# Performance work log

Measured on AMD Instinct MI355X. Metric: run time of the kernel, lower is better.

Reference implementation:

```python
import jax, jax.numpy as jnp
import numpy as np

N_NODES = 50000
N_EDGES = 800000
IN_CH, HID, OUT_CH, N_LAYERS = 512, 64, 40, 64
ALPHA, THETA = 0.5, 1.0


def setup_inputs() -> dict:
    key = jax.random.key(0)
    ks = jax.random.split(key, 6)
    x = jax.random.normal(ks[0], (N_NODES, IN_CH), dtype=jnp.float32)
    edge_index = jax.random.randint(ks[1], (2, N_EDGES), 0, N_NODES, dtype=jnp.int64)
    lin1_w = jax.random.normal(ks[2], (IN_CH, HID), dtype=jnp.float32) * (1.0 / np.sqrt(IN_CH))
    lin1_b = jnp.zeros((HID,), dtype=jnp.float32)
    conv_w = jax.random.normal(ks[3], (N_LAYERS, HID, HID), dtype=jnp.float32) * (1.0 / np.sqrt(HID))
    lin2_w = jax.random.normal(ks[4], (HID, OUT_CH), dtype=jnp.float32) * (1.0 / np.sqrt(HID))
    lin2_b = jnp.zeros((OUT_CH,), dtype=jnp.float32)
    return {"x": x, "edge_index": edge_index, "lin1_w": lin1_w, "lin1_b": lin1_b,
            "conv_w": conv_w, "lin2_w": lin2_w, "lin2_b": lin2_b}


def reference(x, edge_index, lin1_w, lin1_b, conv_w, lin2_w, lin2_b):
    # Eval-mode forward (dropout is identity).
    N = x.shape[0]
    # gcn_norm: add self-loops, symmetric sqrt-degree normalization
    loop = jnp.arange(N, dtype=edge_index.dtype)
    src = jnp.concatenate([edge_index[0], loop])  # [E+N]
    dst = jnp.concatenate([edge_index[1], loop])
    w = jnp.ones(src.shape[0], dtype=x.dtype)
    deg = jax.ops.segment_sum(w, dst, num_segments=N)
    dinv = jnp.where(deg > 0, jax.lax.rsqrt(jnp.maximum(deg, 1e-12)), 0.0)
    norm = (dinv[src] * dinv[dst])[:, None]  # [E+N, 1]

    h = jax.nn.relu(x @ lin1_w + lin1_b)  # [N, HID]
    x0 = h
    L = conv_w.shape[0]
    betas = jnp.log(THETA / jnp.arange(1, L + 1, dtype=x.dtype) + 1.0)

    def step(h, wb):
        W, beta = wb
        # sparse neighbor aggregation: out[i] = sum_{j->i} norm * h[j]
        agg = jax.ops.segment_sum(h[src] * norm, dst, num_segments=N)
        z = (1.0 - ALPHA) * agg + ALPHA * x0            # initial residual
        z = (1.0 - beta) * z + beta * (z @ W)           # identity mapping
        return jax.nn.relu(z), None

    h, _ = jax.lax.scan(step, h, (conv_w, betas))
    out = h @ lin2_w + lin2_b
    return jax.nn.log_softmax(out, axis=1)
```

## Files before the change

### kernel.cpp

```cpp
#include <hip/hip_runtime.h>
#include <hip/hip_bf16.h>
#include <hip/hip_fp16.h>
#include <math.h>

#define HID 64

union HU { __half h; unsigned short u; };
__device__ inline float h2f(unsigned short u) { HU x; x.u = u; return __half2float(x.h); }
__device__ inline unsigned short f2h(float f) { HU x; x.h = __float2half(f); return x.u; }


__global__ void count_kernel(const int* __restrict__ dst, int* __restrict__ cnt, int E, int N) {
    int e = blockIdx.x * blockDim.x + threadIdx.x;
    if (e < E) {
        int d = dst[e];
        if ((unsigned)d < (unsigned)N) atomicAdd(&cnt[d], 1);
    }
}

__global__ void dinv_kernel(const int* __restrict__ cnt, float* __restrict__ dinv, int n) {
    int i = blockIdx.x * blockDim.x + threadIdx.x;
    if (i < n) {
        float deg = (float)(cnt[i] + 1);
        dinv[i] = rsqrtf(deg);
    }
}

__global__ __launch_bounds__(1024) void scanA_kernel(const int* __restrict__ cnt,
        int* __restrict__ offs, int* __restrict__ bsum, int n) {
    __shared__ int buf[1024];
    int tid = threadIdx.x;
    int i = blockIdx.x * 1024 + tid;
    int v = (i < n) ? cnt[i] : 0;
    buf[tid] = v;
    __syncthreads();
    for (int off = 1; off < 1024; off <<= 1) {
        int t = (tid >= off) ? buf[tid - off] : 0;
        __syncthreads();
        buf[tid] += t;
        __syncthreads();
    }
    if (i < n) offs[i] = buf[tid] - v;
    if (tid == 1023) bsum[blockIdx.x] = buf[1023];
}

__global__ __launch_bounds__(1024) void scanB_kernel(int* __restrict__ bsum, int nb) {
    __shared__ int buf[1024];
    int tid = threadIdx.x;
    int v = (tid < nb) ? bsum[tid] : 0;
    buf[tid] = v;
    __syncthreads();
    for (int off = 1; off < 1024; off <<= 1) {
        int t = (tid >= off) ? buf[tid - off] : 0;
        __syncthreads();
        buf[tid] += t;
        __syncthreads();
    }
    if (tid < nb) bsum[tid] = buf[tid] - v;
    if (tid == nb - 1) bsum[nb] = buf[tid];
}

__global__ __launch_bounds__(1024) void scanC_kernel(int* __restrict__ offs,
        const int* __restrict__ bsum, int n, int nb) {
    int i = blockIdx.x * 1024 + threadIdx.x;
    if (i < n) offs[i] += bsum[i >> 10];
    if (i == 0) offs[n] = bsum[nb];
}

__global__ void fill_kernel(const int* __restrict__ src, const int* __restrict__ dst,
                            const int* __restrict__ offs, int* __restrict__ cursor,
                            const float* __restrict__ dinv,
                            int2* __restrict__ pack, int E, int N) {
    int e = blockIdx.x * blockDim.x + threadIdx.x;
    if (e < E) {
        int s = src[e], d = dst[e];
        if ((unsigned)s < (unsigned)N && (unsigned)d < (unsigned)N) {
            int pos = atomicAdd(&cursor[d], 1);
            int j = offs[d] + pos;
            if ((unsigned)j < (unsigned)E)
                pack[j] = make_int2(s, __float_as_int(dinv[s] * dinv[d]));
        }
    }
}


__global__ __launch_bounds__(256) void lin1_kernel(const float* __restrict__ x,
        const float* __restrict__ W, const float* __restrict__ b,
        float* __restrict__ out32, unsigned short* __restrict__ out16, int n) {
    const int BM = 64, BK = 32;
    __shared__ float As[BM][BK + 1];
    __shared__ float Ws[BK][64];
    int tid = threadIdx.x;
    int row0 = blockIdx.x * BM;
    int tx = tid & 15, ty = tid >> 4;
    float acc[4][4] = {};

    int ar = tid >> 3, ac4 = tid & 7;
    int wr = tid >> 4, wc4 = tid & 15;
    float4 a_pf[2], w_pf[2];

    #pragma unroll
    for (int rr = 0; rr < 2; rr++) {
        int row = row0 + ar + rr * 32;
        a_pf[rr] = make_float4(0.f, 0.f, 0.f, 0.f);
        if (row < n) a_pf[rr] = *(const float4*)&x[(size_t)row * 512 + ac4 * 4];
        w_pf[rr] = *(const float4*)&W[(size_t)(wr + rr * 16) * 64 + wc4 * 4];
    }

    for (int k0 = 0; k0 < 512; k0 += BK) {
        #pragma unroll
        for (int rr = 0; rr < 2; rr++) {
            As[ar + rr * 32][ac4 * 4 + 0] = a_pf[rr].x;
            As[ar + rr * 32][ac4 * 4 + 1] = a_pf[rr].y;
            As[ar + rr * 32][ac4 * 4 + 2] = a_pf[rr].z;
            As[ar + rr * 32][ac4 * 4 + 3] = a_pf[rr].w;
            *(float4*)&Ws[wr + rr * 16][wc4 * 4] = w_pf[rr];
        }
        __syncthreads();
        int k1 = k0 + BK;
        if (k1 < 512) {
            #pragma unroll
            for (int rr = 0; rr < 2; rr++) {
                int row = row0 + ar + rr * 32;
                a_pf[rr] = make_float4(0.f, 0.f, 0.f, 0.f);
                if (row < n) a_pf[rr] = *(const float4*)&x[(size_t)row * 512 + k1 + ac4 * 4];
                w_pf[rr] = *(const float4*)&W[(size_t)(k1 + wr + rr * 16) * 64 + wc4 * 4];
            }
        }
        #pragma unroll
        for (int kk = 0; kk < BK; kk++) {
            float a0 = As[ty * 4 + 0][kk];
            float a1 = As[ty * 4 + 1][kk];
            float a2 = As[ty * 4 + 2][kk];
            float a3 = As[ty * 4 + 3][kk];
            float4 w = *(float4*)&Ws[kk][tx * 4];
            acc[0][0] += a0 * w.x; acc[0][1] += a0 * w.y; acc[0][2] += a0 * w.z; acc[0][3] += a0 * w.w;
            acc[1][0] += a1 * w.x; acc[1][1] += a1 * w.y; acc[1][2] += a1 * w.z; acc[1][3] += a1 * w.w;
            acc[2][0] += a2 * w.x; acc[2][1] += a2 * w.y; acc[2][2] += a2 * w.z; acc[2][3] += a2 * w.w;
            acc[3][0] += a3 * w.x; acc[3][1] += a3 * w.y; acc[3][2] += a3 * w.z; acc[3][3] += a3 * w.w;
        }
        __syncthreads();
    }
    #pragma unroll
    for (int i = 0; i < 4; i++) {
        int row = row0 + ty * 4 + i;
        if (row < n) {
            #pragma unroll
            for (int j = 0; j < 4; j++) {
                int col = tx * 4 + j;
                float v = fmaxf(acc[i][j] + b[col], 0.f);
                out32[(size_t)row * 64 + col] = v;
                out16[(size_t)row * 64 + col] = f2h(v);
            }
        }
    }
}


__global__ __launch_bounds__(256) void layer_kernel(
        const ushort4* __restrict__ h16, const float4* __restrict__ x04,
        unsigned short* __restrict__ h_out,
        const int* __restrict__ rowptr, const int2* __restrict__ pack,
        const float* __restrict__ dinv,
        const float* __restrict__ W, float beta, int n) {
    __shared__ float Wsh[HID * HID];
    __shared__ float4 zt[4][HID];
    int tid = threadIdx.x;
    for (int i = tid; i < HID * HID / 4; i += 256)
        ((float4*)Wsh)[i] = ((const float4*)W)[i];
    __syncthreads();
    int lane = tid & 63, wave = tid >> 6;
    int g = lane >> 4;
    int c = lane & 15;
    float omb = 1.0f - beta;

    for (int base = (blockIdx.x * 4 + wave) * 4; base < n; base += gridDim.x * 16) {
        int node = base + g;
        float4 acc = make_float4(0.f, 0.f, 0.f, 0.f);
        if (node < n) {
            float di = dinv[node];
            float d2 = di * di;
            ushort4 sv = h16[(size_t)node * 16 + c];
            acc.x = d2 * h2f(sv.x); acc.y = d2 * h2f(sv.y);
            acc.z = d2 * h2f(sv.z); acc.w = d2 * h2f(sv.w);
            int e0 = rowptr[node];
            int deg = rowptr[node + 1] - e0;
            int e = 0;
            for (; e + 4 <= deg; e += 4) {
                int2 p0 = pack[e0 + e + 0];
                int2 p1 = pack[e0 + e + 1];
                int2 p2 = pack[e0 + e + 2];
                int2 p3 = pack[e0 + e + 3];
                ushort4 v0 = h16[(size_t)p0.x * 16 + c];
                ushort4 v1 = h16[(size_t)p1.x * 16 + c];
                ushort4 v2 = h16[(size_t)p2.x * 16 + c];
                ushort4 v3 = h16[(size_t)p3.x * 16 + c];
                float n0 = __int_as_float(p0.y), n1 = __int_as_float(p1.y);
                float n2 = __int_as_float(p2.y), n3 = __int_as_float(p3.y);
                acc.x += n0 * h2f(v0.x) + n1 * h2f(v1.x) + n2 * h2f(v2.x) + n3 * h2f(v3.x);
                acc.y += n0 * h2f(v0.y) + n1 * h2f(v1.y) + n2 * h2f(v2.y) + n3 * h2f(v3.y);
                acc.z += n0 * h2f(v0.z) + n1 * h2f(v1.z) + n2 * h2f(v2.z) + n3 * h2f(v3.z);
                acc.w += n0 * h2f(v0.w) + n1 * h2f(v1.w) + n2 * h2f(v2.w) + n3 * h2f(v3.w);
            }
            for (; e < deg; e++) {
                int2 p = pack[e0 + e];
                ushort4 v = h16[(size_t)p.x * 16 + c];
                float nv = __int_as_float(p.y);
                acc.x += nv * h2f(v.x); acc.y += nv * h2f(v.y);
                acc.z += nv * h2f(v.z); acc.w += nv * h2f(v.w);
            }
            float4 x0v = x04[(size_t)node * 16 + c];
            acc.x = 0.5f * acc.x + 0.5f * x0v.x;
            acc.y = 0.5f * acc.y + 0.5f * x0v.y;
            acc.z = 0.5f * acc.z + 0.5f * x0v.z;
            acc.w = 0.5f * acc.w + 0.5f * x0v.w;
        }
        {
            float* zf = (float*)&zt[wave][0];
            zf[(4 * c + 0) * 4 + g] = acc.x;
            zf[(4 * c + 1) * 4 + g] = acc.y;
            zf[(4 * c + 2) * 4 + g] = acc.z;
            zf[(4 * c + 3) * 4 + g] = acc.w;
        }
        float4 mv = make_float4(0.f, 0.f, 0.f, 0.f);
        #pragma unroll 8
        for (int k = 0; k < HID; k++) {
            float4 zk = zt[wave][k];
            float wk = Wsh[k * HID + lane];
            mv.x += zk.x * wk; mv.y += zk.y * wk;
            mv.z += zk.z * wk; mv.w += zk.w * wk;
        }
        float4 zrow = zt[wave][lane];
        if (base + 0 < n) h_out[(size_t)(base + 0) * HID + lane] = f2h(fmaxf(omb * zrow.x + beta * mv.x, 0.f));
        if (base + 1 < n) h_out[(size_t)(base + 1) * HID + lane] = f2h(fmaxf(omb * zrow.y + beta * mv.y, 0.f));
        if (base + 2 < n) h_out[(size_t)(base + 2) * HID + lane] = f2h(fmaxf(omb * zrow.z + beta * mv.z, 0.f));
        if (base + 3 < n) h_out[(size_t)(base + 3) * HID + lane] = f2h(fmaxf(omb * zrow.w + beta * mv.w, 0.f));
    }
}


__global__ __launch_bounds__(256) void out_kernel(const unsigned short* __restrict__ h,
        const float* __restrict__ W2, const float* __restrict__ b2,
        float* __restrict__ out, int n) {
    __shared__ float W2s[64 * 40];
    alignas(16) __shared__ float hs[4][64];
    int tid = threadIdx.x;
    for (int i = tid; i < 64 * 40; i += 256) W2s[i] = W2[i];
    __syncthreads();
    int lane = tid & 63, wave = tid >> 6;
    int c = (lane < 40) ? lane : 0;
    float wc[64];
    #pragma unroll
    for (int k = 0; k < 64; k++) wc[k] = W2s[k * 40 + c];
    float bias = b2[c];
    for (int i = blockIdx.x * 4 + wave; i < n; i += gridDim.x * 4) {
        hs[wave][lane] = h2f(h[(size_t)i * 64 + lane]);
        float o = bias;
        #pragma unroll
        for (int k4 = 0; k4 < 16; k4++) {
            float4 hb = *(float4*)&hs[wave][k4 * 4];
            o += hb.x * wc[k4 * 4 + 0] + hb.y * wc[k4 * 4 + 1]
               + hb.z * wc[k4 * 4 + 2] + hb.w * wc[k4 * 4 + 3];
        }
        float val = (lane < 40) ? o : -INFINITY;
        float m = val;
        #pragma unroll
        for (int d = 1; d < 64; d <<= 1) m = fmaxf(m, __shfl_xor(m, d, 64));
        float e = (lane < 40) ? expf(o - m) : 0.f;
        float s = e;
        #pragma unroll
        for (int d = 1; d < 64; d <<= 1) s += __shfl_xor(s, d, 64);
        if (lane < 40) out[(size_t)i * 40 + lane] = (o - m) - logf(s);
    }
}

__global__ void zero_out_kernel(float* __restrict__ out, int n) {
    int i = blockIdx.x * blockDim.x + threadIdx.x;
    if (i < n) out[i] = 0.f;
}


extern "C" void kernel_launch(void* const* d_in, const int* in_sizes, int n_in,
                              void* d_out, int out_size, void* d_ws, size_t ws_size,
                              hipStream_t stream) {
    const float* x    = (const float*)d_in[0];
    const int*   ei   = (const int*)d_in[1];
    const float* W1   = (const float*)d_in[2];
    const float* b1   = (const float*)d_in[3];
    const float* Wc   = (const float*)d_in[4];
    const float* W2   = (const float*)d_in[5];
    const float* b2   = (const float*)d_in[6];
    float* outp = (float*)d_out;

    const int N = in_sizes[0] / 512;
    const int E = in_sizes[1] / 2;
    const int L = in_sizes[4] / (HID * HID);

    const int* src = ei;
    const int* dst = ei + E;
    const int NB_SCAN = (N + 1023) / 1024;

    size_t need = (size_t)N * HID * 4
                + (size_t)N * HID * 2 * 2
                + ((size_t)N * 3 + (N + 1) + (NB_SCAN + 1)) * 4
                + (size_t)E * 8;
    if (ws_size < need) {
        zero_out_kernel<<<(out_size + 255) / 256, 256, 0, stream>>>(outp, out_size);
        return;
    }
    char* p = (char*)d_ws;
    float* x0b  = (float*)p;               p += (size_t)N * HID * 4;
    unsigned short* hA16 = (unsigned short*)p;  p += (size_t)N * HID * 2;
    unsigned short* hB16 = (unsigned short*)p;  p += (size_t)N * HID * 2;
    float* dinv = (float*)p;               p += (size_t)N * 4;
    int2*  pack = (int2*)p;                p += (size_t)E * 8;
    int*   cnt  = (int*)p;                 p += (size_t)N * 4;
    int*   offs = (int*)p;                 p += (size_t)(N + 1) * 4;
    int*   cursor = (int*)p;               p += (size_t)N * 4;
    int*   bsum = (int*)p;                 p += (size_t)(NB_SCAN + 1) * 4;

    hipMemsetAsync(cnt, 0, (size_t)N * 4, stream);
    hipMemsetAsync(cursor, 0, (size_t)N * 4, stream);

    count_kernel<<<(E + 255) / 256, 256, 0, stream>>>(dst, cnt, E, N);
    dinv_kernel<<<(N + 255) / 256, 256, 0, stream>>>(cnt, dinv, N);
    scanA_kernel<<<NB_SCAN, 1024, 0, stream>>>(cnt, offs, bsum, N);
    scanB_kernel<<<1, 1024, 0, stream>>>(bsum, NB_SCAN);
    scanC_kernel<<<NB_SCAN, 1024, 0, stream>>>(offs, bsum, N, NB_SCAN);
    fill_kernel<<<(E + 255) / 256, 256, 0, stream>>>(src, dst, offs, cursor, dinv,
                                                     pack, E, N);

    lin1_kernel<<<(N + 63) / 64, 256, 0, stream>>>(x, W1, b1, x0b, hA16, N);

    unsigned short* cur_in = hA16;
    unsigned short* cur_out = hB16;
    for (int l = 0; l < L; l++) {
        float beta = log1pf(1.0f / (float)(l + 1));
        layer_kernel<<<2048, 256, 0, stream>>>((const ushort4*)cur_in, (const float4*)x0b,
                                               cur_out, offs, pack, dinv,
                                               Wc + (size_t)l * HID * HID, beta, N);
        unsigned short* nxt = cur_in;
        cur_in = cur_out;
        cur_out = nxt;
    }

    out_kernel<<<1024, 256, 0, stream>>>(cur_in, W2, b2, outp, N);
}
```

Measured before the change: 2.198 ms.

## Widen gather to 16-byte loads, 8 nodes per wave, fold beta mix into W

The layer kernel now assigns 8 lanes per node, each loading a full 16-byte chunk (eight halves), so a wave handles 8 nodes instead of 4. The transform is restructured to 8 columns per lane, and the (1-beta)*I + beta*W mix is folded into the shared weight matrix so the epilogue is a plain relu. The grid becomes one block per 32 nodes instead of a fixed 2048 blocks, and lin1 uses a 32-row tile. The intent is fewer, wider gather transactions and more memory-level parallelism, at the cost of more registers per thread and a larger shared-memory z tile.

```diff
diff --git a/kernel.cpp b/kernel.cpp
--- a/kernel.cpp
+++ b/kernel.cpp
@@ -6,8 +6,8 @@
 #define HID 64
 
 union HU { __half h; unsigned short u; };
+__device__ inline unsigned short f2h(float f) { HU x; x.h = __float2half(f); return x.u; }
 __device__ inline float h2f(unsigned short u) { HU x; x.u = u; return __half2float(x.h); }
-__device__ inline unsigned short f2h(float f) { HU x; x.h = __float2half(f); return x.u; }
 
 
 __global__ void count_kernel(const int* __restrict__ dst, int* __restrict__ cnt, int E, int N) {
@@ -87,63 +87,55 @@
 __global__ __launch_bounds__(256) void lin1_kernel(const float* __restrict__ x,
         const float* __restrict__ W, const float* __restrict__ b,
         float* __restrict__ out32, unsigned short* __restrict__ out16, int n) {
-    const int BM = 64, BK = 32;
+    const int BM = 32, BK = 32;
     __shared__ float As[BM][BK + 1];
     __shared__ float Ws[BK][64];
     int tid = threadIdx.x;
     int row0 = blockIdx.x * BM;
     int tx = tid & 15, ty = tid >> 4;
-    float acc[4][4] = {};
+    float acc[2][4] = {};
 
     int ar = tid >> 3, ac4 = tid & 7;
     int wr = tid >> 4, wc4 = tid & 15;
-    float4 a_pf[2], w_pf[2];
-
-    #pragma unroll
-    for (int rr = 0; rr < 2; rr++) {
-        int row = row0 + ar + rr * 32;
-        a_pf[rr] = make_float4(0.f, 0.f, 0.f, 0.f);
-        if (row < n) a_pf[rr] = *(const float4*)&x[(size_t)row * 512 + ac4 * 4];
-        w_pf[rr] = *(const float4*)&W[(size_t)(wr + rr * 16) * 64 + wc4 * 4];
+    float4 a_pf, w_pf0, w_pf1;
+
+    {
+        int row = row0 + ar;
+        a_pf = make_float4(0.f, 0.f, 0.f, 0.f);
+        if (row < n) a_pf = *(const float4*)&x[(size_t)row * 512 + ac4 * 4];
+        w_pf0 = *(const float4*)&W[(size_t)wr * 64 + wc4 * 4];
+        w_pf1 = *(const float4*)&W[(size_t)(wr + 16) * 64 + wc4 * 4];
     }
 
     for (int k0 = 0; k0 < 512; k0 += BK) {
-        #pragma unroll
-        for (int rr = 0; rr < 2; rr++) {
-            As[ar + rr * 32][ac4 * 4 + 0] = a_pf[rr].x;
-            As[ar + rr * 32][ac4 * 4 + 1] = a_pf[rr].y;
-            As[ar + rr * 32][ac4 * 4 + 2] = a_pf[rr].z;
-            As[ar + rr * 32][ac4 * 4 + 3] = a_pf[rr].w;
-            *(float4*)&Ws[wr + rr * 16][wc4 * 4] = w_pf[rr];
-        }
+        As[ar][ac4 * 4 + 0] = a_pf.x;
+        As[ar][ac4 * 4 + 1] = a_pf.y;
+        As[ar][ac4 * 4 + 2] = a_pf.z;
+        As[ar][ac4 * 4 + 3] = a_pf.w;
+        *(float4*)&Ws[wr][wc4 * 4] = w_pf0;
+        *(float4*)&Ws[wr + 16][wc4 * 4] = w_pf1;
         __syncthreads();
         int k1 = k0 + BK;
         if (k1 < 512) {
-            #pragma unroll
-            for (int rr = 0; rr < 2; rr++) {
-                int row = row0 + ar + rr * 32;
-                a_pf[rr] = make_float4(0.f, 0.f, 0.f, 0.f);
-                if (row < n) a_pf[rr] = *(const float4*)&x[(size_t)row * 512 + k1 + ac4 * 4];
-                w_pf[rr] = *(const float4*)&W[(size_t)(k1 + wr + rr * 16) * 64 + wc4 * 4];
-            }
+            int row = row0 + ar;
+            a_pf = make_float4(0.f, 0.f, 0.f, 0.f);
+            if (row < n) a_pf = *(const float4*)&x[(size_t)row * 512 + k1 + ac4 * 4];
+            w_pf0 = *(const float4*)&W[(size_t)(k1 + wr) * 64 + wc4 * 4];
+            w_pf1 = *(const float4*)&W[(size_t)(k1 + wr + 16) * 64 + wc4 * 4];
         }
         #pragma unroll
         for (int kk = 0; kk < BK; kk++) {
-            float a0 = As[ty * 4 + 0][kk];
-            float a1 = As[ty * 4 + 1][kk];
-            float a2 = As[ty * 4 + 2][kk];
-            float a3 = As[ty * 4 + 3][kk];
+            float a0 = As[ty * 2 + 0][kk];
+            float a1 = As[ty * 2 + 1][kk];
             float4 w = *(float4*)&Ws[kk][tx * 4];
             acc[0][0] += a0 * w.x; acc[0][1] += a0 * w.y; acc[0][2] += a0 * w.z; acc[0][3] += a0 * w.w;
             acc[1][0] += a1 * w.x; acc[1][1] += a1 * w.y; acc[1][2] += a1 * w.z; acc[1][3] += a1 * w.w;
-            acc[2][0] += a2 * w.x; acc[2][1] += a2 * w.y; acc[2][2] += a2 * w.z; acc[2][3] += a2 * w.w;
-            acc[3][0] += a3 * w.x; acc[3][1] += a3 * w.y; acc[3][2] += a3 * w.z; acc[3][3] += a3 * w.w;
         }
         __syncthreads();
     }
     #pragma unroll
-    for (int i = 0; i < 4; i++) {
-        int row = row0 + ty * 4 + i;
+    for (int i = 0; i < 2; i++) {
+        int row = row0 + ty * 2 + i;
         if (row < n) {
             #pragma unroll
             for (int j = 0; j < 4; j++) {
@@ -158,31 +150,39 @@
 
 
 __global__ __launch_bounds__(256) void layer_kernel(
-        const ushort4* __restrict__ h16, const float4* __restrict__ x04,
+        const uint4* __restrict__ h16, const float4* __restrict__ x04,
         unsigned short* __restrict__ h_out,
         const int* __restrict__ rowptr, const int2* __restrict__ pack,
         const float* __restrict__ dinv,
         const float* __restrict__ W, float beta, int n) {
     __shared__ float Wsh[HID * HID];
-    __shared__ float4 zt[4][HID];
-    int tid = threadIdx.x;
-    for (int i = tid; i < HID * HID / 4; i += 256)
-        ((float4*)Wsh)[i] = ((const float4*)W)[i];
+    __shared__ float zt[4][HID][8];
+    int tid = threadIdx.x;
+    float omb = 1.0f - beta;
+    for (int i = tid; i < HID * HID; i += 256) {
+        int k = i >> 6, cc = i & 63;
+        Wsh[i] = beta * W[i] + ((k == cc) ? omb : 0.f);
+    }
     __syncthreads();
     int lane = tid & 63, wave = tid >> 6;
-    int g = lane >> 4;
-    int c = lane & 15;
-    float omb = 1.0f - beta;
-
-    for (int base = (blockIdx.x * 4 + wave) * 4; base < n; base += gridDim.x * 16) {
+    int g = lane >> 3;
+    int c = lane & 7;
+
+#define UNPACK_ACC(v, nv)                                              \
+    { float2 q;                                                        \
+      q = __half22float2(*(__half2*)&(v).x); acc[0] += (nv) * q.x; acc[1] += (nv) * q.y; \
+      q = __half22float2(*(__half2*)&(v).y); acc[2] += (nv) * q.x; acc[3] += (nv) * q.y; \
+      q = __half22float2(*(__half2*)&(v).z); acc[4] += (nv) * q.x; acc[5] += (nv) * q.y; \
+      q = __half22float2(*(__half2*)&(v).w); acc[6] += (nv) * q.x; acc[7] += (nv) * q.y; }
+
+    for (int base = (blockIdx.x * 4 + wave) * 8; base < n; base += gridDim.x * 32) {
         int node = base + g;
-        float4 acc = make_float4(0.f, 0.f, 0.f, 0.f);
+        float acc[8] = {0.f, 0.f, 0.f, 0.f, 0.f, 0.f, 0.f, 0.f};
         if (node < n) {
             float di = dinv[node];
             float d2 = di * di;
-            ushort4 sv = h16[(size_t)node * 16 + c];
-            acc.x = d2 * h2f(sv.x); acc.y = d2 * h2f(sv.y);
-            acc.z = d2 * h2f(sv.z); acc.w = d2 * h2f(sv.w);
+            uint4 sv = h16[(size_t)node * 8 + c];
+            UNPACK_ACC(sv, d2);
             int e0 = rowptr[node];
             int deg = rowptr[node + 1] - e0;
             int e = 0;
@@ -191,51 +191,56 @@
                 int2 p1 = pack[e0 + e + 1];
                 int2 p2 = pack[e0 + e + 2];
                 int2 p3 = pack[e0 + e + 3];
-                ushort4 v0 = h16[(size_t)p0.x * 16 + c];
-                ushort4 v1 = h16[(size_t)p1.x * 16 + c];
-                ushort4 v2 = h16[(size_t)p2.x * 16 + c];
-                ushort4 v3 = h16[(size_t)p3.x * 16 + c];
+                uint4 v0 = h16[(size_t)p0.x * 8 + c];
+                uint4 v1 = h16[(size_t)p1.x * 8 + c];
+                uint4 v2 = h16[(size_t)p2.x * 8 + c];
+                uint4 v3 = h16[(size_t)p3.x * 8 + c];
                 float n0 = __int_as_float(p0.y), n1 = __int_as_float(p1.y);
                 float n2 = __int_as_float(p2.y), n3 = __int_as_float(p3.y);
-                acc.x += n0 * h2f(v0.x) + n1 * h2f(v1.x) + n2 * h2f(v2.x) + n3 * h2f(v3.x);
-                acc.y += n0 * h2f(v0.y) + n1 * h2f(v1.y) + n2 * h2f(v2.y) + n3 * h2f(v3.y);
-                acc.z += n0 * h2f(v0.z) + n1 * h2f(v1.z) + n2 * h2f(v2.z) + n3 * h2f(v3.z);
-                acc.w += n0 * h2f(v0.w) + n1 * h2f(v1.w) + n2 * h2f(v2.w) + n3 * h2f(v3.w);
+                UNPACK_ACC(v0, n0);
+                UNPACK_ACC(v1, n1);
+                UNPACK_ACC(v2, n2);
+                UNPACK_ACC(v3, n3);
             }
             for (; e < deg; e++) {
                 int2 p = pack[e0 + e];
-                ushort4 v = h16[(size_t)p.x * 16 + c];
+                uint4 v = h16[(size_t)p.x * 8 + c];
                 float nv = __int_as_float(p.y);
-                acc.x += nv * h2f(v.x); acc.y += nv * h2f(v.y);
-                acc.z += nv * h2f(v.z); acc.w += nv * h2f(v.w);
+                UNPACK_ACC(v, nv);
             }
-            float4 x0v = x04[(size_t)node * 16 + c];
-            acc.x = 0.5f * acc.x + 0.5f * x0v.x;
-            acc.y = 0.5f * acc.y + 0.5f * x0v.y;
-            acc.z = 0.5f * acc.z + 0.5f * x0v.z;
-            acc.w = 0.5f * acc.w + 0.5f * x0v.w;
-        }
-        {
-            float* zf = (float*)&zt[wave][0];
-            zf[(4 * c + 0) * 4 + g] = acc.x;
-            zf[(4 * c + 1) * 4 + g] = acc.y;
-            zf[(4 * c + 2) * 4 + g] = acc.z;
-            zf[(4 * c + 3) * 4 + g] = acc.w;
-        }
-        float4 mv = make_float4(0.f, 0.f, 0.f, 0.f);
-        #pragma unroll 8
+            float4 xa = x04[(size_t)node * 16 + 2 * c];
+            float4 xb = x04[(size_t)node * 16 + 2 * c + 1];
+            acc[0] = 0.5f * acc[0] + 0.5f * xa.x;
+            acc[1] = 0.5f * acc[1] + 0.5f * xa.y;
+            acc[2] = 0.5f * acc[2] + 0.5f * xa.z;
+            acc[3] = 0.5f * acc[3] + 0.5f * xa.w;
+            acc[4] = 0.5f * acc[4] + 0.5f * xb.x;
+            acc[5] = 0.5f * acc[5] + 0.5f * xb.y;
+            acc[6] = 0.5f * acc[6] + 0.5f * xb.z;
+            acc[7] = 0.5f * acc[7] + 0.5f * xb.w;
+        }
+        #pragma unroll
+        for (int j = 0; j < 8; j++)
+            zt[wave][c * 8 + j][g] = acc[j];
+        float mv[8] = {0.f, 0.f, 0.f, 0.f, 0.f, 0.f, 0.f, 0.f};
+        #pragma unroll 4
         for (int k = 0; k < HID; k++) {
-            float4 zk = zt[wave][k];
+            float4 zA = *(float4*)&zt[wave][k][0];
+            float4 zB = *(float4*)&zt[wave][k][4];
             float wk = Wsh[k * HID + lane];
-            mv.x += zk.x * wk; mv.y += zk.y * wk;
-            mv.z += zk.z * wk; mv.w += zk.w * wk;
-        }
-        float4 zrow = zt[wave][lane];
-        if (base + 0 < n) h_out[(size_t)(base + 0) * HID + lane] = f2h(fmaxf(omb * zrow.x + beta * mv.x, 0.f));
-        if (base + 1 < n) h_out[(size_t)(base + 1) * HID + lane] = f2h(fmaxf(omb * zrow.y + beta * mv.y, 0.f));
-        if (base + 2 < n) h_out[(size_t)(base + 2) * HID + lane] = f2h(fmaxf(omb * zrow.z + beta * mv.z, 0.f));
-        if (base + 3 < n) h_out[(size_t)(base + 3) * HID + lane] = f2h(fmaxf(omb * zrow.w + beta * mv.w, 0.f));
-    }
+            mv[0] += zA.x * wk; mv[1] += zA.y * wk;
+            mv[2] += zA.z * wk; mv[3] += zA.w * wk;
+            mv[4] += zB.x * wk; mv[5] += zB.y * wk;
+            mv[6] += zB.z * wk; mv[7] += zB.w * wk;
+        }
+        #pragma unroll
+        for (int j = 0; j < 8; j++) {
+            int row = base + j;
+            if (row < n)
+                h_out[(size_t)row * HID + lane] = f2h(fmaxf(mv[j], 0.f));
+        }
+    }
+#undef UNPACK_ACC
 }
 
 
@@ -330,15 +335,16 @@
     fill_kernel<<<(E + 255) / 256, 256, 0, stream>>>(src, dst, offs, cursor, dinv,
                                                      pack, E, N);
 
-    lin1_kernel<<<(N + 63) / 64, 256, 0, stream>>>(x, W1, b1, x0b, hA16, N);
-
+    lin1_kernel<<<(N + 31) / 32, 256, 0, stream>>>(x, W1, b1, x0b, hA16, N);
+
+    int nblocks = (N + 31) / 32;
     unsigned short* cur_in = hA16;
     unsigned short* cur_out = hB16;
     for (int l = 0; l < L; l++) {
         float beta = log1pf(1.0f / (float)(l + 1));
-        layer_kernel<<<2048, 256, 0, stream>>>((const ushort4*)cur_in, (const float4*)x0b,
-                                               cur_out, offs, pack, dinv,
-                                               Wc + (size_t)l * HID * HID, beta, N);
+        layer_kernel<<<nblocks, 256, 0, stream>>>((const uint4*)cur_in, (const float4*)x0b,
+                                                  cur_out, offs, pack, dinv,
+                                                  Wc + (size_t)l * HID * HID, beta, N);
         unsigned short* nxt = cur_in;
         cur_in = cur_out;
         cur_out = nxt;
```

Measured after the change: 2.207 ms. No clear change (+0.4%).
